# Optimization experiments

Hardware: AMD Instinct MI355X
Metric: run time of the kernel (lower is better)

The kernel has to match this reference:

```python
import jax, jax.numpy as jnp
from jax import lax
import numpy as np

GAMMA = 0.1      # sinkhorn_alpha
EPS = 0.005      # stop_thr
MAXITERS = 1000  # OT_max_iter
TINY = 1e-30


def _pairwise_sq_dist(x, y):
    return (jnp.sum(x * x, axis=1, keepdims=True)
            + jnp.sum(y * y, axis=1)[None, :]
            - 2.0 * (x @ y.T))


def _sinkhorn(M, r, c):
    # M: (B,H,W); r: (1,H); c: (1,W). Faithful to _sinkhorn_inline.
    r_ = r[:, :, None]          # (1,H,1)
    c_ = c[:, None, :]          # (1,W,1 -> 1,1,W)
    M_min = jnp.min(M, axis=2, keepdims=True)
    P0 = jnp.exp(-GAMMA * (M - M_min))

    def cond(state):
        _, err, it = state
        return (err > EPS) & (it < MAXITERS)

    def body(state):
        P, _, it = state
        alpha = jnp.sum(P, axis=2, keepdims=True)
        P1 = P / jnp.maximum(alpha, TINY) * r_
        beta = jnp.sum(P1, axis=1, keepdims=True)
        err = jnp.max(jnp.sum(jnp.abs(beta - c_), axis=2))
        P2 = P1 / jnp.maximum(beta, TINY) * c_
        # torch breaks BEFORE the column update when converged -> keep P1 then
        Pn = jnp.where(err <= EPS, P1, P2)
        return Pn, err, it + 1

    init = (P0, jnp.asarray(jnp.inf, M.dtype), jnp.asarray(0, jnp.int32))
    P, _, _ = lax.while_loop(cond, body, init)
    return P


def setup_inputs() -> dict:
    key = jax.random.key(0)
    k1, k2 = jax.random.split(key)
    x = jax.random.normal(k1, (1024, 512), dtype=jnp.float32)
    y = jax.random.normal(k2, (16384, 512), dtype=jnp.float32)
    return {"x": x, "y": y}


def reference(x, y):
    M = _pairwise_sq_dist(x, y)           # (n, m)
    n, m = M.shape
    # init_a_dist / init_b_dist are None -> uniform marginals (already normalized)
    a = jnp.full((1, n), 1.0 / n, dtype=M.dtype)
    b = jnp.full((1, m), 1.0 / m, dtype=M.dtype)
    # n <= m by construction -> implicit path takes the non-transpose branch
    P = _sinkhorn(M[None], a, b)[0]       # (n, m)
    loss_ETP = jnp.sum(P * M)
    return loss_ETP, P
```

## Files before the change

### kernel.cpp

```cpp
#include <hip/hip_runtime.h>

#define N_ROWS 1024
#define M_COLS 16384
#define DIM 512

constexpr float GAMMA_ = 0.1f;
constexpr float INV_GAMMA = 10.0f;
constexpr float EPS_ = 0.005f;
constexpr float TINY_ = 1e-30f;
constexpr float RVAL = 1.0f / 1024.0f;
constexpr float CVAL = 1.0f / 16384.0f;

typedef __attribute__((ext_vector_type(8))) short bf16x8;
typedef __attribute__((ext_vector_type(4))) float f32x4;

__device__ __forceinline__ float waveRedSum(float v) {
#pragma unroll
    for (int o = 32; o > 0; o >>= 1) v += __shfl_down(v, o);
    return v;
}
__device__ __forceinline__ float waveRedMin(float v) {
#pragma unroll
    for (int o = 32; o > 0; o >>= 1) v = fminf(v, __shfl_down(v, o));
    return v;
}

__device__ __forceinline__ unsigned sysloadu(const unsigned* p) {
    return __hip_atomic_load(p, __ATOMIC_RELAXED, __HIP_MEMORY_SCOPE_SYSTEM);
}
__device__ __forceinline__ void sysstoreu(unsigned* p, unsigned v) {
    __hip_atomic_store(p, v, __ATOMIC_RELAXED, __HIP_MEMORY_SCOPE_SYSTEM);
}
__device__ __forceinline__ float sysloadf(const float* p) {
    return __hip_atomic_load(p, __ATOMIC_RELAXED, __HIP_MEMORY_SCOPE_SYSTEM);
}
__device__ __forceinline__ void sysstoref(float* p, float v) {
    __hip_atomic_store(p, v, __ATOMIC_RELAXED, __HIP_MEMORY_SCOPE_SYSTEM);
}

__device__ __forceinline__ void gbarx(unsigned* __restrict__ arr, unsigned* __restrict__ bcast,
                                      int b, int tid, unsigned e) {
    __syncthreads();
    if (tid == 0) sysstoreu(&arr[b], e);
    if (b == 0) {
        if (tid < 256) {
            while (sysloadu(&arr[tid]) < e) __builtin_amdgcn_s_sleep(1);
        }
        __syncthreads();
        if (tid == 0) sysstoreu(bcast, e);
    } else {
        if (tid == 0) {
            while (sysloadu(bcast) < e) __builtin_amdgcn_s_sleep(1);
        }
    }
    __syncthreads();
}

__global__ void row_sqnorm(const float* __restrict__ X, float* __restrict__ out) {
    int row = blockIdx.x;
    const float* xr = X + (size_t)row * DIM;
    int tid = threadIdx.x;
    float acc = 0.f;
    for (int k = tid; k < DIM; k += 128) { float v = xr[k]; acc = fmaf(v, v, acc); }
    acc = waveRedSum(acc);
    __shared__ float red[2];
    if ((tid & 63) == 0) red[tid >> 6] = acc;
    __syncthreads();
    if (tid == 0) out[row] = red[0] + red[1];
}

__device__ __forceinline__ unsigned bf16b(float f) {
    unsigned u = __float_as_uint(f);
    return (u + 0x7FFFu + ((u >> 16) & 1u)) >> 16;
}

__global__ __launch_bounds__(256, 2) void gemm_dist_mfma(const float* __restrict__ X, const float* __restrict__ Y,
                                                         const float* __restrict__ sx, const float* __restrict__ sy,
                                                         float* __restrict__ Mout) {
    __shared__ __align__(16) char lds[65536];
    char* Ahi = lds;
    char* Alo = lds + 16384;
    char* Bhi = lds + 32768;
    char* Blo = lds + 49152;
    const int tid = threadIdx.x;
    const int lane = tid & 63;
    const int w = tid >> 6;
    const int wm = w >> 1, wn = w & 1;
    const int bid = blockIdx.x;
    const int logical = (bid & 7) * 128 + (bid >> 3);
    const int ct = logical >> 3, rt = logical & 7;
    const int row0 = rt << 7, col0 = ct << 7;

    const int srow = tid >> 2;
    const int squar = tid & 3;

    f32x4 acc[4][4] = {};

    for (int k0 = 0; k0 < DIM; k0 += 64) {
        __syncthreads();
#pragma unroll
        for (int rr = 0; rr < 2; ++rr) {
            const int r = rr * 64 + srow;
            const int swz = (r & 7) << 4;
#pragma unroll
            for (int q = 0; q < 4; ++q) {
                const int kk = squar * 16 + q * 4;
                const int off = (r * 128 + kk * 2) ^ swz;
                {
                    float4 va = *(const float4*)(X + (size_t)(row0 + r) * DIM + k0 + kk);
                    unsigned h0 = bf16b(va.x), h1 = bf16b(va.y), h2 = bf16b(va.z), h3 = bf16b(va.w);
                    float l0f = va.x - __uint_as_float(h0 << 16);
                    float l1f = va.y - __uint_as_float(h1 << 16);
                    float l2f = va.z - __uint_as_float(h2 << 16);
                    float l3f = va.w - __uint_as_float(h3 << 16);
                    *(uint2*)(Ahi + off) = make_uint2(h0 | (h1 << 16), h2 | (h3 << 16));
                    *(uint2*)(Alo + off) = make_uint2(bf16b(l0f) | (bf16b(l1f) << 16),
                                                      bf16b(l2f) | (bf16b(l3f) << 16));
                }
                {
                    float4 vb = *(const float4*)(Y + (size_t)(col0 + r) * DIM + k0 + kk);
                    unsigned h0 = bf16b(vb.x), h1 = bf16b(vb.y), h2 = bf16b(vb.z), h3 = bf16b(vb.w);
                    float l0f = vb.x - __uint_as_float(h0 << 16);
                    float l1f = vb.y - __uint_as_float(h1 << 16);
                    float l2f = vb.z - __uint_as_float(h2 << 16);
                    float l3f = vb.w - __uint_as_float(h3 << 16);
                    *(uint2*)(Bhi + off) = make_uint2(h0 | (h1 << 16), h2 | (h3 << 16));
                    *(uint2*)(Blo + off) = make_uint2(bf16b(l0f) | (bf16b(l1f) << 16),
                                                      bf16b(l2f) | (bf16b(l3f) << 16));
                }
            }
        }
        __syncthreads();
#pragma unroll
        for (int ks = 0; ks < 2; ++ks) {
            const int kb = (ks * 32 + (lane >> 4) * 8) * 2;
            bf16x8 ah[4], al[4], bh[4], bl[4];
#pragma unroll
            for (int i = 0; i < 4; ++i) {
                const int r = wm * 64 + i * 16 + (lane & 15);
                const int offa = (r * 128 + kb) ^ ((r & 7) << 4);
                ah[i] = *(const bf16x8*)(Ahi + offa);
                al[i] = *(const bf16x8*)(Alo + offa);
                const int c = wn * 64 + i * 16 + (lane & 15);
                const int offb = (c * 128 + kb) ^ ((c & 7) << 4);
                bh[i] = *(const bf16x8*)(Bhi + offb);
                bl[i] = *(const bf16x8*)(Blo + offb);
            }
#pragma unroll
            for (int i = 0; i < 4; ++i)
#pragma unroll
                for (int j = 0; j < 4; ++j) {
                    acc[i][j] = __builtin_amdgcn_mfma_f32_16x16x32_bf16(ah[i], bh[j], acc[i][j], 0, 0, 0);
                    acc[i][j] = __builtin_amdgcn_mfma_f32_16x16x32_bf16(ah[i], bl[j], acc[i][j], 0, 0, 0);
                    acc[i][j] = __builtin_amdgcn_mfma_f32_16x16x32_bf16(al[i], bh[j], acc[i][j], 0, 0, 0);
                }
        }
    }
    const int lrow = lane >> 4;
    const int lcol = lane & 15;
#pragma unroll
    for (int i = 0; i < 4; ++i) {
        const int gr0 = row0 + wm * 64 + i * 16 + lrow * 4;
        const float sx0 = sx[gr0], sx1 = sx[gr0 + 1], sx2 = sx[gr0 + 2], sx3 = sx[gr0 + 3];
#pragma unroll
        for (int j = 0; j < 4; ++j) {
            const int gc = col0 + wn * 64 + j * 16 + lcol;
            const float syv = sy[gc];
            float* op = Mout + (size_t)gr0 * M_COLS + gc;
            op[0]                     = sx0 + syv - 2.0f * acc[i][j][0];
            op[(size_t)1 * M_COLS]    = sx1 + syv - 2.0f * acc[i][j][1];
            op[(size_t)2 * M_COLS]    = sx2 + syv - 2.0f * acc[i][j][2];
            op[(size_t)3 * M_COLS]    = sx3 + syv - 2.0f * acc[i][j][3];
        }
    }
}

__global__ void row_min(const float* __restrict__ Mb, float* __restrict__ Mmin) {
    int row = blockIdx.x;
    const float* mr = Mb + (size_t)row * M_COLS;
    int tid = threadIdx.x;
    float mn = INFINITY;
    for (int j = tid; j < M_COLS; j += 256) mn = fminf(mn, mr[j]);
    mn = waveRedMin(mn);
    __shared__ float red[4];
    if ((tid & 63) == 0) red[tid >> 6] = mn;
    __syncthreads();
    if (tid == 0) Mmin[row] = fminf(fminf(red[0], red[1]), fminf(red[2], red[3]));
}

__global__ void init_state(float* __restrict__ ubuf, unsigned* __restrict__ bar,
                           float* __restrict__ out) {
    int idx = blockIdx.x * blockDim.x + threadIdx.x;
    if (idx < 512) bar[idx] = 0u;
    if (idx < 1024) { ubuf[idx] = 1.0f; ubuf[1024 + idx] = 1.0f; }
    if (idx == 0) out[0] = 0.0f;
}

__global__ __launch_bounds__(1024, 4) void sinkhorn_reg(const float* __restrict__ Mmin,
                                                        float* __restrict__ ubuf,
                                                        float* __restrict__ out,
                                                        unsigned* __restrict__ bar) {
    const int tid = threadIdx.x;
    const int b = blockIdx.x;
    const int rg = tid >> 2;
    const int ch = tid & 3;
    const int r0 = rg << 2;
    const int c0 = b << 6;
    float* Pbuf = out + 1;
    float* spart = out + 4;
    float* errpart = out + 4 + 262144;
    unsigned* arr = bar;
    unsigned* bcast = bar + 288;

    __shared__ float v_lds[2][64];
    __shared__ float u_lds[1024];
    __shared__ float t_acc[16][68];
    __shared__ float red[16];
    __shared__ float sh_err;

    if (tid < 64) { v_lds[0][tid] = 1.0f; v_lds[1][tid] = 1.0f; }

    float K[64];
#pragma unroll
    for (int k = 0; k < 4; ++k) {
        const float* mrow = Pbuf + (size_t)(r0 + k) * M_COLS + c0 + ch;
        float mm = Mmin[r0 + k];
#pragma unroll
        for (int c = 0; c < 16; ++c) {
            K[k * 16 + c] = __expf(-GAMMA_ * (mrow[4 * c] - mm));
        }
    }
    gbarx(arr, bcast, b, tid, 1u);

    int cur = 0, vsel = 0, brk = 0;
    unsigned ep = 2u;
    int it = 0;
    for (;; ++it, ep += 2u) {
        {
            float vv[16];
#pragma unroll
            for (int c = 0; c < 16; ++c) vv[c] = v_lds[cur][ch + 4 * c];
            float rs[4];
#pragma unroll
            for (int k = 0; k < 4; ++k) {
                float p = 0.f;
#pragma unroll
                for (int c = 0; c < 16; ++c) p = fmaf(K[k * 16 + c], vv[c], p);
                rs[k] = p;
            }
#pragma unroll
            for (int k = 0; k < 4; ++k) {
                rs[k] += __shfl_xor(rs[k], 1);
                rs[k] += __shfl_xor(rs[k], 2);
            }
            sysstoref(&spart[(size_t)(rg * 256 + b) * 4 + ch], rs[ch]);
        }
        gbarx(arr, bcast, b, tid, ep);
        float* uOld = ubuf + (((it & 1) ^ 1) << 10);
        float* uNew = ubuf + ((it & 1) << 10);
        {
            const int w = tid >> 6, l = tid & 63;
            if (w == 0) {
                float e = 0.f;
                if (it > 0)
                    e = sysloadf(&errpart[l]) + sysloadf(&errpart[l + 64]) +
                        sysloadf(&errpart[l + 128]) + sysloadf(&errpart[l + 192]);
                e = waveRedSum(e);
                if (l == 0) sh_err = (it > 0) ? e : 1e30f;
            } else if (w <= 4) {
                const int k = w - 1;
                const float* sp = spart + ((size_t)b << 10) + k;
                float s = sysloadf(&sp[4 * l]) + sysloadf(&sp[4 * (l + 64)]) +
                          sysloadf(&sp[4 * (l + 128)]) + sysloadf(&sp[4 * (l + 192)]);
                s = waveRedSum(s);
                if (l == 0) {
                    int r = (b << 2) + k;
                    float uo = sysloadf(&uOld[r]);
                    sysstoref(&uNew[r], uo * RVAL / fmaxf(uo * s, TINY_));
                }
            }
        }
        __syncthreads();
        float err = sh_err;
        brk = (err <= EPS_) ? 1 : ((it == 1000) ? 2 : 0);
        gbarx(arr, bcast, b, tid, ep + 1u);
        if (brk) { vsel = (brk == 1) ? (cur ^ 1) : cur; break; }
        if (tid < 256) {
#pragma unroll
            for (int k = 0; k < 4; ++k) u_lds[tid * 4 + k] = sysloadf(&uNew[tid * 4 + k]);
        }
        __syncthreads();
        {
            float uu[4] = {u_lds[r0], u_lds[r0 + 1], u_lds[r0 + 2], u_lds[r0 + 3]};
            float t16[16];
#pragma unroll
            for (int c = 0; c < 16; ++c) {
                float t = 0.f;
#pragma unroll
                for (int k = 0; k < 4; ++k) t = fmaf(K[k * 16 + c], uu[k], t);
                t16[c] = t;
            }
#pragma unroll
            for (int c = 0; c < 16; ++c) {
                t16[c] += __shfl_xor(t16[c], 4);
                t16[c] += __shfl_xor(t16[c], 8);
                t16[c] += __shfl_xor(t16[c], 16);
                t16[c] += __shfl_xor(t16[c], 32);
            }
            const int w = tid >> 6, l = tid & 63;
            if (l < 4) {
#pragma unroll
                for (int c = 0; c < 16; ++c) t_acc[w][l + 4 * c] = t16[c];
            }
        }
        __syncthreads();
        if (tid < 64) {
            float t = 0.f;
#pragma unroll
            for (int w2 = 0; w2 < 16; ++w2) t += t_acc[w2][tid];
            float vc = v_lds[cur][tid];
            float beta = vc * t;
            float e = fabsf(beta - CVAL);
            v_lds[cur ^ 1][tid] = vc * CVAL / fmaxf(beta, TINY_);
            e = waveRedSum(e);
            if (tid == 0) sysstoref(&errpart[b], e);
        }
        __syncthreads();
        cur ^= 1;
    }

    const float* uEpi = ubuf + (((it & 1) ^ 1) << 10);
    float vv[16];
#pragma unroll
    for (int c = 0; c < 16; ++c) vv[c] = v_lds[vsel][ch + 4 * c];
    float uu[4];
#pragma unroll
    for (int k = 0; k < 4; ++k) uu[k] = sysloadf(&uEpi[r0 + k]);
    float4 mm4 = *(const float4*)(Mmin + r0);
    float mm[4] = {mm4.x, mm4.y, mm4.z, mm4.w};
    float lsum = 0.f;
#pragma unroll
    for (int k = 0; k < 4; ++k) {
        float* prow = Pbuf + (size_t)(r0 + k) * M_COLS + c0 + ch;
#pragma unroll
        for (int c = 0; c < 16; ++c) {
            float kv = K[k * 16 + c];
            float p = 0.f;
            if (kv > 0.f) {
                p = uu[k] * kv * vv[c];
                float m = mm[k] - __logf(kv) * INV_GAMMA;
                lsum = fmaf(p, m, lsum);
            }
            prow[4 * c] = p;
        }
    }
    lsum = waveRedSum(lsum);
    if ((tid & 63) == 0) red[tid >> 6] = lsum;
    __syncthreads();
    if (tid == 0) {
        float s = 0.f;
#pragma unroll
        for (int i = 0; i < 16; ++i) s += red[i];
        atomicAdd(out, s);
    }
}

extern "C" void kernel_launch(void* const* d_in, const int* in_sizes, int n_in,
                              void* d_out, int out_size, void* d_ws, size_t ws_size,
                              hipStream_t stream) {
    const float* x = (const float*)d_in[0];
    const float* y = (const float*)d_in[1];
    float* out = (float*)d_out;
    float* P = out + 1;
    float* ws = (float*)d_ws;
    float* sx   = ws;
    float* sy   = ws + 1024;
    float* Mmin = ws + 17408;
    float* ubuf = ws + 18432;
    unsigned* bar = (unsigned*)(ws + 20480);

    row_sqnorm<<<N_ROWS, 128, 0, stream>>>(x, sx);
    row_sqnorm<<<M_COLS, 128, 0, stream>>>(y, sy);
    init_state<<<4, 256, 0, stream>>>(ubuf, bar, out);
    gemm_dist_mfma<<<1024, 256, 0, stream>>>(x, y, sx, sy, P);
    row_min<<<N_ROWS, 256, 0, stream>>>(P, Mmin);
    {
        const float* Mminc = Mmin;
        void* args[] = {(void*)&Mminc, (void*)&ubuf, (void*)&out, (void*)&bar};
        hipLaunchCooperativeKernel((const void*)sinkhorn_reg, dim3(256), dim3(1024), args, 0, stream);
    }
}
```

Baseline: 258.2 us.

## Fuse row-min into GEMM epilogue and flatten grid barrier to all-poll

The separate row-min kernel is removed. The GEMM epilogue computes per-row minima with wave shuffles and atomicMin on an order-preserving unsigned key, avoiding a second full pass over the distance matrix. The grid barrier drops the block-0 broadcast stage and has every block poll all arrival slots, removing one latency hop per barrier. This adds global atomics in the GEMM and more polling traffic on barrier counters.

```diff
diff --git a/kernel.cpp b/kernel.cpp
--- a/kernel.cpp
+++ b/kernel.cpp
@@ -19,10 +19,14 @@
     for (int o = 32; o > 0; o >>= 1) v += __shfl_down(v, o);
     return v;
 }
-__device__ __forceinline__ float waveRedMin(float v) {
-#pragma unroll
-    for (int o = 32; o > 0; o >>= 1) v = fminf(v, __shfl_down(v, o));
-    return v;
+
+__device__ __forceinline__ unsigned fkey(float x) {
+    unsigned u = __float_as_uint(x);
+    return (u & 0x80000000u) ? ~u : (u | 0x80000000u);
+}
+__device__ __forceinline__ float fdec(unsigned k) {
+    unsigned u = (k & 0x80000000u) ? (k & 0x7FFFFFFFu) : ~k;
+    return __uint_as_float(u);
 }
 
 __device__ __forceinline__ unsigned sysloadu(const unsigned* p) {
@@ -38,20 +42,11 @@
     __hip_atomic_store(p, v, __ATOMIC_RELAXED, __HIP_MEMORY_SCOPE_SYSTEM);
 }
 
-__device__ __forceinline__ void gbarx(unsigned* __restrict__ arr, unsigned* __restrict__ bcast,
-                                      int b, int tid, unsigned e) {
+__device__ __forceinline__ void gbarx(unsigned* __restrict__ arr, int b, int tid, unsigned e) {
     __syncthreads();
     if (tid == 0) sysstoreu(&arr[b], e);
-    if (b == 0) {
-        if (tid < 256) {
-            while (sysloadu(&arr[tid]) < e) __builtin_amdgcn_s_sleep(1);
-        }
-        __syncthreads();
-        if (tid == 0) sysstoreu(bcast, e);
-    } else {
-        if (tid == 0) {
-            while (sysloadu(bcast) < e) __builtin_amdgcn_s_sleep(1);
-        }
+    if (tid < 256) {
+        while (sysloadu(&arr[tid]) < e) __builtin_amdgcn_s_sleep(1);
     }
     __syncthreads();
 }
@@ -76,7 +71,7 @@
 
 __global__ __launch_bounds__(256, 2) void gemm_dist_mfma(const float* __restrict__ X, const float* __restrict__ Y,
                                                          const float* __restrict__ sx, const float* __restrict__ sy,
-                                                         float* __restrict__ Mout) {
+                                                         float* __restrict__ Mout, unsigned* __restrict__ MminKey) {
     __shared__ __align__(16) char lds[65536];
     char* Ahi = lds;
     char* Alo = lds + 16384;
@@ -162,41 +157,48 @@
     for (int i = 0; i < 4; ++i) {
         const int gr0 = row0 + wm * 64 + i * 16 + lrow * 4;
         const float sx0 = sx[gr0], sx1 = sx[gr0 + 1], sx2 = sx[gr0 + 2], sx3 = sx[gr0 + 3];
+        float rmn0 = 1e30f, rmn1 = 1e30f, rmn2 = 1e30f, rmn3 = 1e30f;
 #pragma unroll
         for (int j = 0; j < 4; ++j) {
             const int gc = col0 + wn * 64 + j * 16 + lcol;
             const float syv = sy[gc];
             float* op = Mout + (size_t)gr0 * M_COLS + gc;
-            op[0]                     = sx0 + syv - 2.0f * acc[i][j][0];
-            op[(size_t)1 * M_COLS]    = sx1 + syv - 2.0f * acc[i][j][1];
-            op[(size_t)2 * M_COLS]    = sx2 + syv - 2.0f * acc[i][j][2];
-            op[(size_t)3 * M_COLS]    = sx3 + syv - 2.0f * acc[i][j][3];
-        }
-    }
-}
-
-__global__ void row_min(const float* __restrict__ Mb, float* __restrict__ Mmin) {
-    int row = blockIdx.x;
-    const float* mr = Mb + (size_t)row * M_COLS;
-    int tid = threadIdx.x;
-    float mn = INFINITY;
-    for (int j = tid; j < M_COLS; j += 256) mn = fminf(mn, mr[j]);
-    mn = waveRedMin(mn);
-    __shared__ float red[4];
-    if ((tid & 63) == 0) red[tid >> 6] = mn;
-    __syncthreads();
-    if (tid == 0) Mmin[row] = fminf(fminf(red[0], red[1]), fminf(red[2], red[3]));
+            float m0 = sx0 + syv - 2.0f * acc[i][j][0];
+            float m1 = sx1 + syv - 2.0f * acc[i][j][1];
+            float m2 = sx2 + syv - 2.0f * acc[i][j][2];
+            float m3 = sx3 + syv - 2.0f * acc[i][j][3];
+            op[0]                  = m0;
+            op[(size_t)1 * M_COLS] = m1;
+            op[(size_t)2 * M_COLS] = m2;
+            op[(size_t)3 * M_COLS] = m3;
+            rmn0 = fminf(rmn0, m0); rmn1 = fminf(rmn1, m1);
+            rmn2 = fminf(rmn2, m2); rmn3 = fminf(rmn3, m3);
+        }
+#pragma unroll
+        for (int o = 1; o < 16; o <<= 1) {
+            rmn0 = fminf(rmn0, __shfl_xor(rmn0, o));
+            rmn1 = fminf(rmn1, __shfl_xor(rmn1, o));
+            rmn2 = fminf(rmn2, __shfl_xor(rmn2, o));
+            rmn3 = fminf(rmn3, __shfl_xor(rmn3, o));
+        }
+        if (lcol == 0) {
+            atomicMin(&MminKey[gr0 + 0], fkey(rmn0));
+            atomicMin(&MminKey[gr0 + 1], fkey(rmn1));
+            atomicMin(&MminKey[gr0 + 2], fkey(rmn2));
+            atomicMin(&MminKey[gr0 + 3], fkey(rmn3));
+        }
+    }
 }
 
 __global__ void init_state(float* __restrict__ ubuf, unsigned* __restrict__ bar,
-                           float* __restrict__ out) {
+                           unsigned* __restrict__ MminKey, float* __restrict__ out) {
     int idx = blockIdx.x * blockDim.x + threadIdx.x;
     if (idx < 512) bar[idx] = 0u;
-    if (idx < 1024) { ubuf[idx] = 1.0f; ubuf[1024 + idx] = 1.0f; }
+    if (idx < 1024) { ubuf[idx] = 1.0f; ubuf[1024 + idx] = 1.0f; MminKey[idx] = 0xFFFFFFFFu; }
     if (idx == 0) out[0] = 0.0f;
 }
 
-__global__ __launch_bounds__(1024, 4) void sinkhorn_reg(const float* __restrict__ Mmin,
+__global__ __launch_bounds__(1024, 4) void sinkhorn_reg(const unsigned* __restrict__ MminKey,
                                                         float* __restrict__ ubuf,
                                                         float* __restrict__ out,
                                                         unsigned* __restrict__ bar) {
@@ -210,7 +212,6 @@
     float* spart = out + 4;
     float* errpart = out + 4 + 262144;
     unsigned* arr = bar;
-    unsigned* bcast = bar + 288;
 
     __shared__ float v_lds[2][64];
     __shared__ float u_lds[1024];
@@ -224,13 +225,13 @@
 #pragma unroll
     for (int k = 0; k < 4; ++k) {
         const float* mrow = Pbuf + (size_t)(r0 + k) * M_COLS + c0 + ch;
-        float mm = Mmin[r0 + k];
+        float mm = fdec(MminKey[r0 + k]);
 #pragma unroll
         for (int c = 0; c < 16; ++c) {
             K[k * 16 + c] = __expf(-GAMMA_ * (mrow[4 * c] - mm));
         }
     }
-    gbarx(arr, bcast, b, tid, 1u);
+    gbarx(arr, b, tid, 1u);
 
     int cur = 0, vsel = 0, brk = 0;
     unsigned ep = 2u;
@@ -255,7 +256,7 @@
             }
             sysstoref(&spart[(size_t)(rg * 256 + b) * 4 + ch], rs[ch]);
         }
-        gbarx(arr, bcast, b, tid, ep);
+        gbarx(arr, b, tid, ep);
         float* uOld = ubuf + (((it & 1) ^ 1) << 10);
         float* uNew = ubuf + ((it & 1) << 10);
         {
@@ -283,7 +284,7 @@
         __syncthreads();
         float err = sh_err;
         brk = (err <= EPS_) ? 1 : ((it == 1000) ? 2 : 0);
-        gbarx(arr, bcast, b, tid, ep + 1u);
+        gbarx(arr, b, tid, ep + 1u);
         if (brk) { vsel = (brk == 1) ? (cur ^ 1) : cur; break; }
         if (tid < 256) {
 #pragma unroll
@@ -336,8 +337,9 @@
     float uu[4];
 #pragma unroll
     for (int k = 0; k < 4; ++k) uu[k] = sysloadf(&uEpi[r0 + k]);
-    float4 mm4 = *(const float4*)(Mmin + r0);
-    float mm[4] = {mm4.x, mm4.y, mm4.z, mm4.w};
+    float mm[4];
+#pragma unroll
+    for (int k = 0; k < 4; ++k) mm[k] = fdec(MminKey[r0 + k]);
     float lsum = 0.f;
 #pragma unroll
     for (int k = 0; k < 4; ++k) {
@@ -375,18 +377,17 @@
     float* ws = (float*)d_ws;
     float* sx   = ws;
     float* sy   = ws + 1024;
-    float* Mmin = ws + 17408;
+    unsigned* MminKey = (unsigned*)(ws + 17408);
     float* ubuf = ws + 18432;
     unsigned* bar = (unsigned*)(ws + 20480);
 
     row_sqnorm<<<N_ROWS, 128, 0, stream>>>(x, sx);
     row_sqnorm<<<M_COLS, 128, 0, stream>>>(y, sy);
-    init_state<<<4, 256, 0, stream>>>(ubuf, bar, out);
-    gemm_dist_mfma<<<1024, 256, 0, stream>>>(x, y, sx, sy, P);
-    row_min<<<N_ROWS, 256, 0, stream>>>(P, Mmin);
+    init_state<<<4, 256, 0, stream>>>(ubuf, bar, MminKey, out);
+    gemm_dist_mfma<<<1024, 256, 0, stream>>>(x, y, sx, sy, P, MminKey);
     {
-        const float* Mminc = Mmin;
-        void* args[] = {(void*)&Mminc, (void*)&ubuf, (void*)&out, (void*)&bar};
+        const unsigned* Mk = MminKey;
+        void* args[] = {(void*)&Mk, (void*)&ubuf, (void*)&out, (void*)&bar};
         hipLaunchCooperativeKernel((const void*)sinkhorn_reg, dim3(256), dim3(1024), args, 0, stream);
     }
 }
```

Result: slower. 289.8 us (+12.2%).
